# Performance work log

Hardware: AMD Instinct MI355X
Metric: run time of the kernel (lower is better)

## Reference

```python
import jax, jax.numpy as jnp
import numpy as np

B, H, W, C = 16, 32, 32, 512
L, CT = 77, 512
NH, HD = 8, 64
G = 32          # GroupNorm groups
EPS = 1e-6      # flax GroupNorm default epsilon
NEG = -1e10


def group_norm(x, scale, bias):
    # flax GroupNorm on [b, n, c]: stats over (n, channels-within-group) per (b, group)
    b, n, c = x.shape
    xg = x.reshape(b, n, G, c // G)
    mu = xg.mean(axis=(1, 3), keepdims=True)
    var = xg.var(axis=(1, 3), keepdims=True)
    xg = (xg - mu) * jax.lax.rsqrt(var + EPS)
    return xg.reshape(b, n, c) * scale + bias


def setup_inputs() -> dict:
    key = jax.random.key(0)
    ks = jax.random.split(key, 8)
    w = lambda k, shape: jax.random.normal(k, shape, jnp.float32) * 0.02
    return {
        "inputs": jax.random.normal(ks[0], (B, H, W, C), jnp.float32),
        "text_enc": jax.random.normal(ks[1], (B, L, CT), jnp.float32),
        "text_mask": jnp.ones((B, L), jnp.int32),
        "gn_q_scale": jnp.ones((C,), jnp.float32),
        "gn_q_bias": jnp.zeros((C,), jnp.float32),
        "gn_kv_scale": jnp.ones((C,), jnp.float32),
        "gn_kv_bias": jnp.zeros((C,), jnp.float32),
        "gn_t_scale": jnp.ones((CT,), jnp.float32),
        "gn_t_bias": jnp.zeros((CT,), jnp.float32),
        "Wq": w(ks[2], (C, NH, HD)),
        "Wk_self": w(ks[3], (C, NH, HD)),
        "Wv_self": w(ks[4], (C, NH, HD)),
        "Wk_cross": w(ks[5], (CT, NH, HD)),
        "Wv_cross": w(ks[6], (CT, NH, HD)),
        "Wout": w(ks[7], (NH, HD, C)),
    }


def reference(inputs, text_enc, text_mask,
              gn_q_scale, gn_q_bias, gn_kv_scale, gn_kv_bias,
              gn_t_scale, gn_t_bias,
              Wq, Wk_self, Wv_self, Wk_cross, Wv_cross, Wout):
    b, h, w, c = inputs.shape
    n = h * w
    x = inputs.reshape(b, n, c)

    x_q = group_norm(x, gn_q_scale, gn_q_bias)
    x_kv = group_norm(x, gn_kv_scale, gn_kv_bias)
    t = group_norm(text_enc, gn_t_scale, gn_t_bias)

    # q/k/v projections; fused: KV = concat(self-KV from image, cross-KV from text)
    scale = jnp.asarray(1.0 / np.sqrt(HD), inputs.dtype)
    q = jnp.einsum('bqc,chd->bqhd', x_q, Wq) * scale  # scale_attn_logits
    k = jnp.concatenate([jnp.einsum('bkc,chd->bkhd', x_kv, Wk_self),
                         jnp.einsum('blc,chd->blhd', t, Wk_cross)], axis=1)
    v = jnp.concatenate([jnp.einsum('bkc,chd->bkhd', x_kv, Wv_self),
                         jnp.einsum('blc,chd->blhd', t, Wv_cross)], axis=1)

    # make_attention_mask(ones[b,n], concat(ones[b,n], text_mask)) -> [b,1,n,n+l];
    # query mask is all ones so only the KV mask matters.
    kv_mask = jnp.concatenate(
        [jnp.ones((b, n), jnp.bool_), text_mask > 0], axis=1)  # [b, n+l]

    logits = jnp.einsum('bqhd,bkhd->bhqk', q, k)  # [b, nh, n, n+l]
    logits = jnp.where(kv_mask[:, None, None, :], logits, jnp.asarray(NEG, logits.dtype))
    probs = jax.nn.softmax(logits, axis=-1)
    attn = jnp.einsum('bhqk,bkhd->bqhd', probs, v)
    out = jnp.einsum('bqhd,hdc->bqc', attn, Wout)
    return out.reshape(b, h, w, c) + inputs
```

## Files before the change

kernel.cpp:

```cpp
#include <hip/hip_runtime.h>
#include <hip/hip_bf16.h>

typedef __hip_bfloat16 bf16;
typedef __attribute__((ext_vector_type(8))) short short8;
typedef __attribute__((ext_vector_type(4))) float f32x4;
typedef __attribute__((ext_vector_type(16))) float f32x16;
#define MFMA16(a, b, c) __builtin_amdgcn_mfma_f32_16x16x32_bf16(a, b, c, 0, 0, 0)
#define MFMA32(a, b, c) __builtin_amdgcn_mfma_f32_32x32x16_bf16(a, b, c, 0, 0, 0)

#define BB   16
#define CCH  512
#define NN   1024
#define LLT  77
#define LPAD 128
#define NHH  8
#define HDD  64
#define GGN  32
#define NKV  1101
#define KVP  1152

__device__ __forceinline__ unsigned short f2bu(float f){
  bf16 h = __float2bfloat16(f);
  return *reinterpret_cast<unsigned short*>(&h);
}

__device__ __forceinline__ unsigned pk2(float lo, float hi){
  unsigned r;
  asm("v_cvt_pk_bf16_f32 %0, %1, %2" : "=v"(r) : "v"(lo), "v"(hi));
  return r;
}

__device__ __forceinline__ float fexp2(float x){
  float r;
  asm("v_exp_f32 %0, %1" : "=v"(r) : "v"(x));
  return r;
}

__device__ __forceinline__ void pl32swap(unsigned &a, unsigned &b){
  asm("v_permlane32_swap_b32 %0, %1" : "+v"(a), "+v"(b));
}

__device__ __forceinline__ void gload16(const bf16* g, bf16* l){
  __builtin_amdgcn_global_load_lds(
      (const __attribute__((address_space(1))) unsigned int*)g,
      (__attribute__((address_space(3))) unsigned int*)l,
      16, 0, 0);
}

__global__ __launch_bounds__(256) void pre_kernel(
    const float* __restrict__ ximg, const float* __restrict__ xtxt,
    float* __restrict__ stats,
    const float* __restrict__ W0, const float* __restrict__ W1,
    const float* __restrict__ W2, const float* __restrict__ W3,
    const float* __restrict__ W4, const float* __restrict__ W5,
    bf16* __restrict__ Wt)
{
  __shared__ float sh1[256], sh2[256];
  __shared__ alignas(16) float Ws[64][68];

  if (blockIdx.x < 1024){
    int isimg = blockIdx.x < 512;
    int bid = blockIdx.x & 511;
    int b = bid >> 5, g = bid & 31;
    int npos = isimg ? NN : LLT;
    const float* xb = (isimg ? ximg : xtxt) + (size_t)b * npos * CCH + g * 16;
    int tot4 = npos * 4;
    float s = 0.f, s2 = 0.f;
    for (int e = threadIdx.x; e < tot4; e += 256){
      int n = e >> 2, cq = (e & 3) * 4;
      float4 v = *(const float4*)(xb + (size_t)n * CCH + cq);
      s  += v.x + v.y + v.z + v.w;
      s2 += v.x * v.x + v.y * v.y + v.z * v.z + v.w * v.w;
    }
    sh1[threadIdx.x] = s; sh2[threadIdx.x] = s2;
    __syncthreads();
    for (int off = 128; off > 0; off >>= 1){
      if (threadIdx.x < off){
        sh1[threadIdx.x] += sh1[threadIdx.x + off];
        sh2[threadIdx.x] += sh2[threadIdx.x + off];
      }
      __syncthreads();
    }
    if (threadIdx.x == 0){
      float inv = 1.f / (float)(npos * 16);
      float m = sh1[0] * inv;
      float var = sh2[0] * inv - m * m;
      float* mu = stats + (isimg ? 0 : 1024);
      mu[bid] = m;
      mu[512 + bid] = rsqrtf(var + 1e-6f);
    }
  } else {
    int i = blockIdx.x - 1024;
    int wsel = i >> 6;
    int rem  = i & 63;
    int n0 = (rem & 7) * 64, k0 = (rem >> 3) * 64;
    const float* W = wsel == 0 ? W0 : wsel == 1 ? W1 : wsel == 2 ? W2 :
                     wsel == 3 ? W3 : wsel == 4 ? W4 : W5;
    bf16* dst = Wt + (size_t)wsel * CCH * CCH;

    int r = threadIdx.x >> 2, c = (threadIdx.x & 3) * 16;
    const float* src = W + (size_t)(k0 + r) * CCH + n0 + c;
    *(float4*)&Ws[r][c]      = *(const float4*)(src);
    *(float4*)&Ws[r][c + 4]  = *(const float4*)(src + 4);
    *(float4*)&Ws[r][c + 8]  = *(const float4*)(src + 8);
    *(float4*)&Ws[r][c + 12] = *(const float4*)(src + 12);
    __syncthreads();

    int nr = threadIdx.x >> 2, kc = (threadIdx.x & 3) * 16;
    uint4 o0, o1;
    o0.x = pk2(Ws[kc + 0][nr],  Ws[kc + 1][nr]);
    o0.y = pk2(Ws[kc + 2][nr],  Ws[kc + 3][nr]);
    o0.z = pk2(Ws[kc + 4][nr],  Ws[kc + 5][nr]);
    o0.w = pk2(Ws[kc + 6][nr],  Ws[kc + 7][nr]);
    o1.x = pk2(Ws[kc + 8][nr],  Ws[kc + 9][nr]);
    o1.y = pk2(Ws[kc + 10][nr], Ws[kc + 11][nr]);
    o1.z = pk2(Ws[kc + 12][nr], Ws[kc + 13][nr]);
    o1.w = pk2(Ws[kc + 14][nr], Ws[kc + 15][nr]);
    bf16* d = dst + (size_t)(n0 + nr) * CCH + k0 + kc;
    *(uint4*)d = o0;
    *(uint4*)(d + 8) = o1;
  }
}

__global__ __launch_bounds__(256) void norm_all_kernel(
    const float* __restrict__ x, const float* __restrict__ t,
    const float* __restrict__ stats,
    const float* __restrict__ gqs, const float* __restrict__ gqb,
    const float* __restrict__ gks, const float* __restrict__ gkb,
    const float* __restrict__ gts, const float* __restrict__ gtb,
    bf16* __restrict__ Xq, bf16* __restrict__ Xkv, bf16* __restrict__ Tn)
{
  if (blockIdx.x < 4096){
    size_t e = ((size_t)blockIdx.x * 256 + threadIdx.x) * 8;
    int b  = (int)(e >> 19);
    int ch = (int)(e & 511);
    int g  = ch >> 4;
    float m = stats[b * GGN + g], r = stats[512 + b * GGN + g];
    float4 x0 = *(const float4*)(x + e);
    float4 x1 = *(const float4*)(x + e + 4);
    float4 sq0 = *(const float4*)(gqs + ch), sq1 = *(const float4*)(gqs + ch + 4);
    float4 bq0 = *(const float4*)(gqb + ch), bq1 = *(const float4*)(gqb + ch + 4);
    float4 sk0 = *(const float4*)(gks + ch), sk1 = *(const float4*)(gks + ch + 4);
    float4 bk0 = *(const float4*)(gkb + ch), bk1 = *(const float4*)(gkb + ch + 4);
    float xs[8] = {x0.x,x0.y,x0.z,x0.w,x1.x,x1.y,x1.z,x1.w};
    float sqv[8] = {sq0.x,sq0.y,sq0.z,sq0.w,sq1.x,sq1.y,sq1.z,sq1.w};
    float bqv[8] = {bq0.x,bq0.y,bq0.z,bq0.w,bq1.x,bq1.y,bq1.z,bq1.w};
    float skv[8] = {sk0.x,sk0.y,sk0.z,sk0.w,sk1.x,sk1.y,sk1.z,sk1.w};
    float bkv[8] = {bk0.x,bk0.y,bk0.z,bk0.w,bk1.x,bk1.y,bk1.z,bk1.w};
    float q[8], k[8];
    #pragma unroll
    for (int j = 0; j < 8; j++){
      float nx = (xs[j] - m) * r;
      q[j] = (nx * sqv[j] + bqv[j]) * 0.18033688f;
      k[j] = nx * skv[j] + bkv[j];
    }
    uint4 oq, ok;
    oq.x = pk2(q[0], q[1]); oq.y = pk2(q[2], q[3]);
    oq.z = pk2(q[4], q[5]); oq.w = pk2(q[6], q[7]);
    ok.x = pk2(k[0], k[1]); ok.y = pk2(k[2], k[3]);
    ok.z = pk2(k[4], k[5]); ok.w = pk2(k[6], k[7]);
    *(uint4*)(Xq + e)  = oq;
    *(uint4*)(Xkv + e) = ok;
  } else {
    size_t e = ((size_t)(blockIdx.x - 4096) * 256 + threadIdx.x) * 8;
    int b  = (int)(e >> 16);
    int rem = (int)(e & 65535);
    int l  = rem >> 9;
    int ch = rem & 511;
    uint4 o;
    if (l < LLT){
      int g = ch >> 4;
      float m = stats[1024 + b * GGN + g], r = stats[1536 + b * GGN + g];
      const float* src = t + ((size_t)b * LLT + l) * CCH + ch;
      float4 x0 = *(const float4*)src, x1 = *(const float4*)(src + 4);
      float4 s0 = *(const float4*)(gts + ch), s1 = *(const float4*)(gts + ch + 4);
      float4 b0 = *(const float4*)(gtb + ch), b1 = *(const float4*)(gtb + ch + 4);
      float xs[8] = {x0.x,x0.y,x0.z,x0.w,x1.x,x1.y,x1.z,x1.w};
      float sv[8] = {s0.x,s0.y,s0.z,s0.w,s1.x,s1.y,s1.z,s1.w};
      float bv[8] = {b0.x,b0.y,b0.z,b0.w,b1.x,b1.y,b1.z,b1.w};
      float w[8];
      #pragma unroll
      for (int j = 0; j < 8; j++) w[j] = (xs[j] - m) * r * sv[j] + bv[j];
      o.x = pk2(w[0], w[1]); o.y = pk2(w[2], w[3]);
      o.z = pk2(w[4], w[5]); o.w = pk2(w[6], w[7]);
    } else {
      o = make_uint4(0, 0, 0, 0);
    }
    *(uint4*)(Tn + e) = o;
  }
}

__global__ __launch_bounds__(256) void proj_all_mfma(
    const bf16* __restrict__ Xq, const bf16* __restrict__ Xkv,
    const bf16* __restrict__ Tn, const bf16* __restrict__ Wt,
    bf16* __restrict__ Qo, bf16* __restrict__ Ko, bf16* __restrict__ Vo)
{
  __shared__ alignas(16) char SHRAW[65536];
  const int tid  = threadIdx.x;
  const int wave = tid >> 6, lane = tid & 63;
  const int l16 = lane & 15, quad = lane >> 4;
  const int bx = blockIdx.x;

  if (bx < 1536){
    bf16 (*T)[4][64][64] = reinterpret_cast<bf16(*)[4][64][64]>(SHRAW);
    const int wr = wave >> 1, wc = wave & 1;
    const int ct = bx >> 7;
    const int rt = bx & 127;
    const int mat = ct >> 2;
    const int cm0 = (ct & 3) * 128;
    const int b  = rt >> 3;
    const int n0 = (rt & 7) * 128;

    const bf16* A  = (mat == 0) ? Xq : Xkv;
    const bf16* Bw = Wt + (size_t)mat * CCH * CCH + (size_t)cm0 * CCH;

    f32x4 acc[4][4];
    #pragma unroll
    for (int rf = 0; rf < 4; rf++)
      #pragma unroll
      for (int cf = 0; cf < 4; cf++) acc[rf][cf] = (f32x4){0.f,0.f,0.f,0.f};

    const int lrow = lane >> 3, lcol = (lane & 7) * 8;
    const bf16* srcbase = (wave < 2)
        ? A  + ((size_t)b * NN + n0 + wave * 64) * CCH
        : Bw + (size_t)((wave - 2) * 64) * CCH;

    #pragma unroll
    for (int c = 0; c < 8; c++)
      gload16(srcbase + (size_t)(c * 8 + lrow) * CCH + lcol, &T[0][wave][c * 8][0]);
    __syncthreads();

    int cur = 0;
    for (int kt = 0; kt < 8; kt++){
      if (kt < 7){
        const int kc = (kt + 1) * 64;
        #pragma unroll
        for (int c = 0; c < 8; c++)
          gload16(srcbase + (size_t)(c * 8 + lrow) * CCH + kc + lcol,
                  &T[cur ^ 1][wave][c * 8][0]);
      }

      short8 af[4][2];
      #pragma unroll
      for (int rf = 0; rf < 4; rf++){
        af[rf][0] = *(const short8*)&T[cur][wr][rf * 16 + l16][quad * 8];
        af[rf][1] = *(const short8*)&T[cur][wr][rf * 16 + l16][32 + quad * 8];
      }
      #pragma unroll
      for (int cf = 0; cf < 4; cf++){
        const short8 b0 = *(const short8*)&T[cur][2 + wc][cf * 16 + l16][quad * 8];
        const short8 b1 = *(const short8*)&T[cur][2 + wc][cf * 16 + l16][32 + quad * 8];
        #pragma unroll
        for (int rf = 0; rf < 4; rf++){
          acc[rf][cf] = MFMA16(af[rf][0], b0, acc[rf][cf]);
          acc[rf][cf] = MFMA16(af[rf][1], b1, acc[rf][cf]);
        }
      }
      __syncthreads();
      cur ^= 1;
    }

    const int h  = (cm0 + wc * 64) >> 6;
    const int nb = n0 + wr * 64;
    bf16 (*Tw)[64] = reinterpret_cast<bf16(*)[64]>(SHRAW + wave * 8192);

    if (mat < 2){
      bf16* Out = (mat == 0) ? Qo : Ko;
      const int stride = (mat == 0) ? NN : KVP;
      #pragma unroll
      for (int rf = 0; rf < 4; rf++)
        #pragma unroll
        for (int cf = 0; cf < 4; cf++)
          #pragma unroll
          for (int r = 0; r < 4; r++)
            Tw[rf * 16 + quad * 4 + r][cf * 16 + l16] =
                __float2bfloat16(acc[rf][cf][r]);
      const int rr = lane >> 2, cs = (lane & 3) * 16;
      #pragma unroll
      for (int k2 = 0; k2 < 4; k2++){
        const int row = rr + k2 * 16;
        bf16* od = Out + (((size_t)b * NHH + h) * stride + nb + row) * HDD + cs;
        *(uint4*)od       = *(const uint4*)&Tw[row][cs];
        *(uint4*)(od + 8) = *(const uint4*)&Tw[row][cs + 8];
      }
    } else {
      #pragma unroll
      for (int cf = 0; cf < 4; cf++)
        #pragma unroll
        for (int rf = 0; rf < 4; rf++)
          #pragma unroll
          for (int r = 0; r < 4; r++)
            Tw[cf * 16 + l16][rf * 16 + quad * 4 + r] =
                __float2bfloat16(acc[rf][cf][r]);
      __syncthreads();
      const int dl = lane >> 2, cseg = (lane & 3) * 16;
      #pragma unroll
      for (int k2 = 0; k2 < 4; k2++){
        const int d = dl + k2 * 16;
        bf16* vd = Vo + (((size_t)b * NHH + h) * HDD + d) * KVP + nb + cseg;
        *(uint4*)vd       = *(const uint4*)&Tw[d][cseg];
        *(uint4*)(vd + 8) = *(const uint4*)&Tw[d][cseg + 8];
      }
    }
  } else {
    bf16 (*At)[72] = reinterpret_cast<bf16(*)[72]>(SHRAW);
    bf16 (*Bk)[72] = reinterpret_cast<bf16(*)[72]>(SHRAW + 64 * 72 * 2);
    bf16 (*Bv)[72] = reinterpret_cast<bf16(*)[72]>(SHRAW + 2 * 64 * 72 * 2);
    const int i  = bx - 1536;
    const int h  = i & 7;
    const int l0 = ((i >> 3) & 1) * 64;
    const int b  = i >> 4;

    const bf16* Wkc = Wt + 3 * (size_t)CCH * CCH;
    const bf16* Wvc = Wt + 4 * (size_t)CCH * CCH;

    f32x4 sk[4], sv[4];
    #pragma unroll
    for (int nt = 0; nt < 4; nt++){
      sk[nt] = (f32x4){0.f,0.f,0.f,0.f};
      sv[nt] = (f32x4){0.f,0.f,0.f,0.f};
    }

    const int sr = tid >> 2, sc = (tid & 3) * 16;
    const bf16* p_a  = Tn  + ((size_t)b * LPAD + l0 + sr) * CCH + sc;
    const bf16* p_bk = Wkc + (size_t)(h * 64 + sr) * CCH + sc;
    const bf16* p_bv = Wvc + (size_t)(h * 64 + sr) * CCH + sc;

    uint4 ra0 = *(const uint4*)p_a,   ra1 = *(const uint4*)(p_a + 8);
    uint4 rk0 = *(const uint4*)p_bk,  rk1 = *(const uint4*)(p_bk + 8);
    uint4 rv0 = *(const uint4*)p_bv,  rv1 = *(const uint4*)(p_bv + 8);

    for (int kt = 0; kt < 8; kt++){
      *(uint4*)&At[sr][sc]     = ra0;  *(uint4*)&At[sr][sc + 8] = ra1;
      *(uint4*)&Bk[sr][sc]     = rk0;  *(uint4*)&Bk[sr][sc + 8] = rk1;
      *(uint4*)&Bv[sr][sc]     = rv0;  *(uint4*)&Bv[sr][sc + 8] = rv1;
      if (kt < 7){
        const int k1 = (kt + 1) * 64;
        ra0 = *(const uint4*)(p_a + k1);   ra1 = *(const uint4*)(p_a + k1 + 8);
        rk0 = *(const uint4*)(p_bk + k1);  rk1 = *(const uint4*)(p_bk + k1 + 8);
        rv0 = *(const uint4*)(p_bv + k1);  rv1 = *(const uint4*)(p_bv + k1 + 8);
      }
      __syncthreads();

      const short8 a0 = *(const short8*)&At[wave * 16 + l16][quad * 8];
      const short8 a1 = *(const short8*)&At[wave * 16 + l16][32 + quad * 8];
      #pragma unroll
      for (int nt = 0; nt < 4; nt++){
        const short8 bk0 = *(const short8*)&Bk[nt * 16 + l16][quad * 8];
        const short8 bk1 = *(const short8*)&Bk[nt * 16 + l16][32 + quad * 8];
        sk[nt] = MFMA16(a0, bk0, sk[nt]);
        sk[nt] = MFMA16(a1, bk1, sk[nt]);
        const short8 bv0 = *(const short8*)&Bv[nt * 16 + l16][quad * 8];
        const short8 bv1 = *(const short8*)&Bv[nt * 16 + l16][32 + quad * 8];
        sv[nt] = MFMA16(a0, bv0, sv[nt]);
        sv[nt] = MFMA16(a1, bv1, sv[nt]);
      }
      __syncthreads();
    }

    #pragma unroll
    for (int r = 0; r < 4; r++){
      int kvrow = NN + l0 + wave * 16 + quad * 4 + r;
      bf16* kd = Ko + (((size_t)b * NHH + h) * KVP + kvrow) * HDD + l16;
      #pragma unroll
      for (int nt = 0; nt < 4; nt++)
        kd[nt * 16] = __float2bfloat16(sk[nt][r]);
    }

    __syncthreads();
    #pragma unroll
    for (int nt = 0; nt < 4; nt++)
      #pragma unroll
      for (int r = 0; r < 4; r++)
        Bk[nt * 16 + l16][wave * 16 + quad * 4 + r] = __float2bfloat16(sv[nt][r]);
    __syncthreads();
    {
      int d = tid >> 2, c = (tid & 3) * 16;
      bf16* vd = Vo + (((size_t)b * NHH + h) * HDD + d) * KVP + NN + l0 + c;
      *(uint4*)vd       = *(const uint4*)&Bk[d][c];
      *(uint4*)(vd + 8) = *(const uint4*)&Bk[d][c + 8];
    }
  }
}

__global__ __launch_bounds__(256, 4) void attn_mfma_kernel(
    const bf16* __restrict__ Q, const bf16* __restrict__ K,
    const bf16* __restrict__ Vt, const int* __restrict__ tmask,
    bf16* __restrict__ Ao)
{
  const int tid  = threadIdx.x;
  const int wave = tid >> 6;
  const int lane = tid & 63;
  const int l31  = lane & 31;
  const int hi   = lane >> 5;
  const int bx = blockIdx.x;
  const int q0 = (bx >> 7) * 128;
  const int g  = bx & 127;
  const int h  = g & 7;
  const int b  = g >> 3;

  __shared__ alignas(16) bf16 KV[2][2][64][72];

  const bf16* qp = Q + (((size_t)b * NHH + h) * NN + q0 + wave * 32 + l31) * HDD + hi * 8;
  short8 qf[4];
  qf[0] = *(const short8*)(qp);
  qf[1] = *(const short8*)(qp + 16);
  qf[2] = *(const short8*)(qp + 32);
  qf[3] = *(const short8*)(qp + 48);

  union { unsigned u[4]; short8 s8; } ones;
  ones.u[0] = 0x3F803F80u; ones.u[1] = 0x3F803F80u;
  ones.u[2] = 0x3F803F80u; ones.u[3] = 0x3F803F80u;

  f32x16 zf;
  #pragma unroll
  for (int i = 0; i < 16; i++) zf[i] = 0.f;

  f32x16 o_acc[2], l_acc;
  #pragma unroll
  for (int dt = 0; dt < 2; dt++)
    #pragma unroll
    for (int i = 0; i < 16; i++) o_acc[dt][i] = 0.f;
  #pragma unroll
  for (int i = 0; i < 16; i++) l_acc[i] = 0.f;

  const size_t kbase = ((size_t)b * NHH + h) * KVP;
  const size_t vbase = ((size_t)b * NHH + h) * (size_t)HDD * KVP;

  const int sr = tid >> 2;
  const int sc = (tid & 3) * 16;
  const bf16* kp = K  + (kbase + sr) * HDD + sc;
  const bf16* vp = Vt + vbase + (size_t)sr * KVP + sc;

  uint4 kr0 = *(const uint4*)kp, kr1 = *(const uint4*)(kp + 8);
  uint4 vr0 = *(const uint4*)vp, vr1 = *(const uint4*)(vp + 8);
  *(uint4*)&KV[0][0][sr][sc]     = kr0;
  *(uint4*)&KV[0][0][sr][sc + 8] = kr1;
  *(uint4*)&KV[0][1][sr][sc]     = vr0;
  *(uint4*)&KV[0][1][sr][sc + 8] = vr1;
  kr0 = *(const uint4*)(kp + 4096); kr1 = *(const uint4*)(kp + 4096 + 8);
  vr0 = *(const uint4*)(vp + 64);   vr1 = *(const uint4*)(vp + 64 + 8);
  __syncthreads();

  for (int kt = 0; kt < 18; kt++){
    const int cur = kt & 1;
    if (kt + 1 < 18){
      *(uint4*)&KV[cur ^ 1][0][sr][sc]     = kr0;
      *(uint4*)&KV[cur ^ 1][0][sr][sc + 8] = kr1;
      *(uint4*)&KV[cur ^ 1][1][sr][sc]     = vr0;
      *(uint4*)&KV[cur ^ 1][1][sr][sc + 8] = vr1;
    }
    if (kt + 2 < 18){
      const size_t ko = (size_t)(kt + 2) * 4096;
      const int    vo = (kt + 2) * 64;
      kr0 = *(const uint4*)(kp + ko); kr1 = *(const uint4*)(kp + ko + 8);
      vr0 = *(const uint4*)(vp + vo); vr1 = *(const uint4*)(vp + vo + 8);
    }

    const bf16 (*Ks)[72] = KV[cur][0];
    const bf16 (*Vs)[72] = KV[cur][1];
    const int kv0 = kt * 64;

    #pragma unroll
    for (int t = 0; t < 2; t++){
      const short8 kf0 = *(const short8*)&Ks[t * 32 + l31][hi * 8];
      const short8 kf1 = *(const short8*)&Ks[t * 32 + l31][16 + hi * 8];
      const short8 kf2 = *(const short8*)&Ks[t * 32 + l31][32 + hi * 8];
      const short8 kf3 = *(const short8*)&Ks[t * 32 + l31][48 + hi * 8];
      __builtin_amdgcn_s_setprio(1);
      f32x16 s = MFMA32(kf0, qf[0], zf);
      s = MFMA32(kf1, qf[1], s);
      s = MFMA32(kf2, qf[2], s);
      s = MFMA32(kf3, qf[3], s);
      __builtin_amdgcn_s_setprio(0);

      if (kv0 + 64 > NN){
        #pragma unroll
        for (int r = 0; r < 16; r++){
          int idx = kv0 - NN + t * 32 + (r & 3) + 8 * (r >> 2) + 4 * hi;
          int ci = idx < LLT ? idx : LLT - 1;
          float rep = (idx < LLT)
                        ? (tmask[b * LLT + ci] > 0 ? 1e30f : -1e10f)
                        : -1e30f;
          s[r] = fminf(s[r], rep);
        }
      }

      #pragma unroll
      for (int r = 0; r < 16; r++) s[r] = fexp2(s[r]);

      unsigned w0 = pk2(s[0],  s[1]),  w1 = pk2(s[2],  s[3]);
      unsigned w2 = pk2(s[4],  s[5]),  w3 = pk2(s[6],  s[7]);
      unsigned w4 = pk2(s[8],  s[9]),  w5 = pk2(s[10], s[11]);
      unsigned w6 = pk2(s[12], s[13]), w7 = pk2(s[14], s[15]);
      pl32swap(w0, w2);
      pl32swap(w1, w3);
      pl32swap(w4, w6);
      pl32swap(w5, w7);
      union { unsigned u[4]; short8 s8; } pf0, pf1;
      pf0.u[0] = w0; pf0.u[1] = w1; pf0.u[2] = w2; pf0.u[3] = w3;
      pf1.u[0] = w4; pf1.u[1] = w5; pf1.u[2] = w6; pf1.u[3] = w7;

      const short8 vf00 = *(const short8*)&Vs[l31][t * 32 + hi * 8];
      const short8 vf01 = *(const short8*)&Vs[l31][t * 32 + 16 + hi * 8];
      const short8 vf10 = *(const short8*)&Vs[32 + l31][t * 32 + hi * 8];
      const short8 vf11 = *(const short8*)&Vs[32 + l31][t * 32 + 16 + hi * 8];

      __builtin_amdgcn_s_setprio(1);
      l_acc = MFMA32(pf0.s8, ones.s8, l_acc);
      l_acc = MFMA32(pf1.s8, ones.s8, l_acc);
      o_acc[0] = MFMA32(pf0.s8, vf00, o_acc[0]);
      o_acc[0] = MFMA32(pf1.s8, vf01, o_acc[0]);
      o_acc[1] = MFMA32(pf0.s8, vf10, o_acc[1]);
      o_acc[1] = MFMA32(pf1.s8, vf11, o_acc[1]);
      __builtin_amdgcn_s_setprio(0);
    }
    __syncthreads();
  }

  #pragma unroll
  for (int r = 0; r < 16; r++){
    const int ql = (r & 3) + 8 * (r >> 2) + 4 * hi;
    const float linv = 1.f / l_acc[r];
    const int n = q0 + wave * 32 + ql;
    bf16* dst = Ao + ((size_t)b * NN + n) * CCH + h * HDD + l31;
    dst[0]  = __float2bfloat16(o_acc[0][r] * linv);
    dst[32] = __float2bfloat16(o_acc[1][r] * linv);
  }
}

__global__ __launch_bounds__(256) void outproj_mfma(
    const bf16* __restrict__ A, const bf16* __restrict__ Wt,
    const float* __restrict__ resid, float* __restrict__ out)
{
  __shared__ alignas(16) char SH[36864];
  bf16 (*T)[64][64] = reinterpret_cast<bf16(*)[64][64]>(SH);
  const int tid  = threadIdx.x;
  const int wave = tid >> 6, lane = tid & 63;
  const int l16 = lane & 15, quad = lane >> 4;
  const int wr = wave >> 1, wc = wave & 1;
  const int bx = blockIdx.x;
  const int c0 = (bx >> 7) * 128;
  const int g0 = (bx & 127) * 128;

  const bf16* Bw = Wt + (size_t)5 * CCH * CCH + (size_t)c0 * CCH;

  f32x4 acc[4][4];
  #pragma unroll
  for (int rf = 0; rf < 4; rf++)
    #pragma unroll
    for (int cf = 0; cf < 4; cf++) acc[rf][cf] = (f32x4){0.f,0.f,0.f,0.f};

  const int lrow = lane >> 3, lcol = (lane & 7) * 8;
  const bf16* srcbase = (wave < 2)
      ? A  + ((size_t)g0 + wave * 64) * CCH
      : Bw + (size_t)((wave - 2) * 64) * CCH;

  for (int kt = 0; kt < 8; kt++){
    const int kc = kt * 64;
    #pragma unroll
    for (int c = 0; c < 8; c++){
      const bf16* g = srcbase + (size_t)(c * 8 + lrow) * CCH + kc + lcol;
      gload16(g, &T[wave][c * 8][0]);
    }
    __syncthreads();

    short8 af[4][2];
    #pragma unroll
    for (int rf = 0; rf < 4; rf++){
      af[rf][0] = *(const short8*)&T[wr][rf * 16 + l16][quad * 8];
      af[rf][1] = *(const short8*)&T[wr][rf * 16 + l16][32 + quad * 8];
    }
    #pragma unroll
    for (int cf = 0; cf < 4; cf++){
      const short8 b0 = *(const short8*)&T[2 + wc][cf * 16 + l16][quad * 8];
      const short8 b1 = *(const short8*)&T[2 + wc][cf * 16 + l16][32 + quad * 8];
      #pragma unroll
      for (int rf = 0; rf < 4; rf++){
        acc[rf][cf] = MFMA16(af[rf][0], b0, acc[rf][cf]);
        acc[rf][cf] = MFMA16(af[rf][1], b1, acc[rf][cf]);
      }
    }
    __syncthreads();
  }

  float (*Tf)[68] = reinterpret_cast<float(*)[68]>(SH + wave * 8704);
  const int cg = (lane & 15) * 4;
  #pragma unroll
  for (int hf = 0; hf < 2; hf++){
    #pragma unroll
    for (int rf = 0; rf < 2; rf++)
      #pragma unroll
      for (int cf = 0; cf < 4; cf++)
        #pragma unroll
        for (int r = 0; r < 4; r++)
          Tf[rf * 16 + quad * 4 + r][cf * 16 + l16] = acc[hf * 2 + rf][cf][r];
    #pragma unroll
    for (int k = 0; k < 8; k++){
      const int row32 = k * 4 + quad;
      const size_t grow = (size_t)g0 + wr * 64 + hf * 32 + row32;
      const int gcol = c0 + wc * 64 + cg;
      float4 v  = *(const float4*)&Tf[row32][cg];
      float4 rz = *(const float4*)&resid[grow * CCH + gcol];
      v.x += rz.x; v.y += rz.y; v.z += rz.z; v.w += rz.w;
      *(float4*)&out[grow * CCH + gcol] = v;
    }
    if (hf == 0){
      asm volatile("s_waitcnt lgkmcnt(0)" ::: "memory");
      __builtin_amdgcn_sched_barrier(0);
    }
  }
}

extern "C" void kernel_launch(void* const* d_in, const int* in_sizes, int n_in,
                              void* d_out, int out_size, void* d_ws, size_t ws_size,
                              hipStream_t stream)
{
  const float* x     = (const float*)d_in[0];
  const float* txt   = (const float*)d_in[1];
  const int*   tmask = (const int*)d_in[2];
  const float* gqs   = (const float*)d_in[3];
  const float* gqb   = (const float*)d_in[4];
  const float* gks   = (const float*)d_in[5];
  const float* gkb   = (const float*)d_in[6];
  const float* gts   = (const float*)d_in[7];
  const float* gtb   = (const float*)d_in[8];
  const float* Wq    = (const float*)d_in[9];
  const float* Wks   = (const float*)d_in[10];
  const float* Wvs   = (const float*)d_in[11];
  const float* Wkc   = (const float*)d_in[12];
  const float* Wvc   = (const float*)d_in[13];
  const float* Wout  = (const float*)d_in[14];

  float* stats = (float*)d_ws;
  bf16* WtAll = (bf16*)(stats + 2048);
  bf16* Xq  = WtAll + (size_t)6 * CCH * CCH;
  bf16* Xkv = Xq  + (size_t)BB * NN * CCH;
  bf16* Tn  = Xkv + (size_t)BB * NN * CCH;
  bf16* Qw  = Tn  + (size_t)BB * LPAD * CCH;
  bf16* Kw  = Qw  + (size_t)BB * NHH * NN * HDD;
  bf16* Vw  = Kw  + (size_t)BB * NHH * KVP * HDD;
  bf16* Aw  = Xq;

  pre_kernel<<<1408, 256, 0, stream>>>(
      x, txt, stats, Wq, Wks, Wvs, Wkc, Wvc, Wout, WtAll);
  norm_all_kernel<<<4608, 256, 0, stream>>>(
      x, txt, stats, gqs, gqb, gks, gkb, gts, gtb, Xq, Xkv, Tn);
  proj_all_mfma<<<1792, 256, 0, stream>>>(
      Xq, Xkv, Tn, WtAll, Qw, Kw, Vw);
  attn_mfma_kernel<<<1024, 256, 0, stream>>>(Qw, Kw, Vw, tmask, Aw);
  outproj_mfma<<<512, 256, 0, stream>>>(Aw, WtAll, x, (float*)d_out);
}
```

Measured before the change: 241.7 us.

## Fuse GroupNorm statistics and normalization into one kernel per group

Merges the stats pass and the elementwise normalize pass into a single kernel: each block computes its (batch, group) mean and rstd, then re-reads its group's slice and writes the bf16 Xq/Xkv/Tn outputs. This removes one kernel launch and the global stats round trip, and the second read of x is likely to hit cache. In exchange the normalize pass runs on only 512 blocks with strided 16-channel slices and 8-byte stores, which lowers parallelism and coalescing compared with the old 4096-block fully contiguous pass.

```diff
diff --git a/kernel.cpp b/kernel.cpp
--- a/kernel.cpp
+++ b/kernel.cpp
@@ -18,6 +18,7 @@
 #define GGN  32
 #define NKV  1101
 #define KVP  1152
+#define QSC  0.18033688f
 
 __device__ __forceinline__ unsigned short f2bu(float f){
   bf16 h = __float2bfloat16(f);
@@ -47,66 +48,121 @@
       16, 0, 0);
 }
 
-__global__ __launch_bounds__(256) void pre_kernel(
-    const float* __restrict__ ximg, const float* __restrict__ xtxt,
-    float* __restrict__ stats,
+__global__ __launch_bounds__(256) void gn_norm_kernel(
+    const float* __restrict__ x, const float* __restrict__ t,
+    const float* __restrict__ gqs, const float* __restrict__ gqb,
+    const float* __restrict__ gks, const float* __restrict__ gkb,
+    const float* __restrict__ gts, const float* __restrict__ gtb,
     const float* __restrict__ W0, const float* __restrict__ W1,
     const float* __restrict__ W2, const float* __restrict__ W3,
     const float* __restrict__ W4, const float* __restrict__ W5,
-    bf16* __restrict__ Wt)
+    bf16* __restrict__ Wt,
+    bf16* __restrict__ Xq, bf16* __restrict__ Xkv, bf16* __restrict__ Tn)
 {
-  __shared__ float sh1[256], sh2[256];
+  __shared__ float sh1[256], sh2[256], mr[2];
   __shared__ alignas(16) float Ws[64][68];
-
-  if (blockIdx.x < 1024){
-    int isimg = blockIdx.x < 512;
-    int bid = blockIdx.x & 511;
-    int b = bid >> 5, g = bid & 31;
-    int npos = isimg ? NN : LLT;
-    const float* xb = (isimg ? ximg : xtxt) + (size_t)b * npos * CCH + g * 16;
-    int tot4 = npos * 4;
+  const int tid = threadIdx.x;
+  const int bid = blockIdx.x;
+
+  if (bid < 512){
+    const int b = bid >> 5, g = bid & 31;
+    const float* xb = x + (size_t)b * NN * CCH + g * 16;
     float s = 0.f, s2 = 0.f;
-    for (int e = threadIdx.x; e < tot4; e += 256){
-      int n = e >> 2, cq = (e & 3) * 4;
+    for (int i = tid; i < 4096; i += 256){
+      const int n = i >> 2, cq = (i & 3) * 4;
       float4 v = *(const float4*)(xb + (size_t)n * CCH + cq);
       s  += v.x + v.y + v.z + v.w;
       s2 += v.x * v.x + v.y * v.y + v.z * v.z + v.w * v.w;
     }
-    sh1[threadIdx.x] = s; sh2[threadIdx.x] = s2;
+    sh1[tid] = s; sh2[tid] = s2;
     __syncthreads();
     for (int off = 128; off > 0; off >>= 1){
-      if (threadIdx.x < off){
-        sh1[threadIdx.x] += sh1[threadIdx.x + off];
-        sh2[threadIdx.x] += sh2[threadIdx.x + off];
-      }
+      if (tid < off){ sh1[tid] += sh1[tid + off]; sh2[tid] += sh2[tid + off]; }
       __syncthreads();
     }
-    if (threadIdx.x == 0){
-      float inv = 1.f / (float)(npos * 16);
-      float m = sh1[0] * inv;
-      float var = sh2[0] * inv - m * m;
-      float* mu = stats + (isimg ? 0 : 1024);
-      mu[bid] = m;
-      mu[512 + bid] = rsqrtf(var + 1e-6f);
+    if (tid == 0){
+      const float inv = 1.f / 16384.f;
+      const float m = sh1[0] * inv;
+      mr[0] = m;
+      mr[1] = rsqrtf(sh2[0] * inv - m * m + 1e-6f);
+    }
+    __syncthreads();
+    const float m = mr[0], r = mr[1];
+    const int ch0 = g * 16;
+    for (int i = tid; i < 4096; i += 256){
+      const int n = i >> 2, cq = (i & 3) * 4;
+      const int ch = ch0 + cq;
+      float4 v  = *(const float4*)(xb + (size_t)n * CCH + cq);
+      float4 sq = *(const float4*)(gqs + ch), bq = *(const float4*)(gqb + ch);
+      float4 sk = *(const float4*)(gks + ch), bk = *(const float4*)(gkb + ch);
+      const float n0 = (v.x - m) * r, n1 = (v.y - m) * r;
+      const float n2 = (v.z - m) * r, n3 = (v.w - m) * r;
+      uint2 oq, ok;
+      oq.x = pk2((n0 * sq.x + bq.x) * QSC, (n1 * sq.y + bq.y) * QSC);
+      oq.y = pk2((n2 * sq.z + bq.z) * QSC, (n3 * sq.w + bq.w) * QSC);
+      ok.x = pk2(n0 * sk.x + bk.x, n1 * sk.y + bk.y);
+      ok.y = pk2(n2 * sk.z + bk.z, n3 * sk.w + bk.w);
+      const size_t off = ((size_t)b * NN + n) * CCH + ch;
+      *(uint2*)(Xq  + off) = oq;
+      *(uint2*)(Xkv + off) = ok;
+    }
+  } else if (bid < 1024){
+    const int b = (bid - 512) >> 5, g = (bid - 512) & 31;
+    const float* tb = t + (size_t)b * LLT * CCH + g * 16;
+    float s = 0.f, s2 = 0.f;
+    for (int i = tid; i < 308; i += 256){
+      const int l = i >> 2, cq = (i & 3) * 4;
+      float4 v = *(const float4*)(tb + (size_t)l * CCH + cq);
+      s  += v.x + v.y + v.z + v.w;
+      s2 += v.x * v.x + v.y * v.y + v.z * v.z + v.w * v.w;
+    }
+    sh1[tid] = s; sh2[tid] = s2;
+    __syncthreads();
+    for (int off = 128; off > 0; off >>= 1){
+      if (tid < off){ sh1[tid] += sh1[tid + off]; sh2[tid] += sh2[tid + off]; }
+      __syncthreads();
+    }
+    if (tid == 0){
+      const float inv = 1.f / (float)(LLT * 16);
+      const float m = sh1[0] * inv;
+      mr[0] = m;
+      mr[1] = rsqrtf(sh2[0] * inv - m * m + 1e-6f);
+    }
+    __syncthreads();
+    const float m = mr[0], r = mr[1];
+    const int ch0 = g * 16;
+    for (int i = tid; i < 512; i += 256){
+      const int l = i >> 2, cq = (i & 3) * 4;
+      const int ch = ch0 + cq;
+      uint2 o;
+      if (l < LLT){
+        float4 v  = *(const float4*)(tb + (size_t)l * CCH + cq);
+        float4 sv = *(const float4*)(gts + ch), bv = *(const float4*)(gtb + ch);
+        o.x = pk2((v.x - m) * r * sv.x + bv.x, (v.y - m) * r * sv.y + bv.y);
+        o.y = pk2((v.z - m) * r * sv.z + bv.z, (v.w - m) * r * sv.w + bv.w);
+      } else {
+        o.x = 0u; o.y = 0u;
+      }
+      *(uint2*)(Tn + ((size_t)b * LPAD + l) * CCH + ch) = o;
     }
   } else {
-    int i = blockIdx.x - 1024;
-    int wsel = i >> 6;
-    int rem  = i & 63;
-    int n0 = (rem & 7) * 64, k0 = (rem >> 3) * 64;
+    const int i = bid - 1024;
+    const int wsel = i >> 6;
+    const int rem  = i & 63;
+    const int n0 = (rem & 7) * 64, k0 = (rem >> 3) * 64;
     const float* W = wsel == 0 ? W0 : wsel == 1 ? W1 : wsel == 2 ? W2 :
                      wsel == 3 ? W3 : wsel == 4 ? W4 : W5;
     bf16* dst = Wt + (size_t)wsel * CCH * CCH;
 
-    int r = threadIdx.x >> 2, c = (threadIdx.x & 3) * 16;
-    const float* src = W + (size_t)(k0 + r) * CCH + n0 + c;
-    *(float4*)&Ws[r][c]      = *(const float4*)(src);
-    *(float4*)&Ws[r][c + 4]  = *(const float4*)(src + 4);
-    *(float4*)&Ws[r][c + 8]  = *(const float4*)(src + 8);
-    *(float4*)&Ws[r][c + 12] = *(const float4*)(src + 12);
-    __syncthreads();
-
-    int nr = threadIdx.x >> 2, kc = (threadIdx.x & 3) * 16;
+    const int rr = tid >> 2, c = (tid & 3) * 16;
+    const float* src = W + (size_t)(k0 + rr) * CCH + n0 + c;
+    *(float4*)&Ws[rr][c]      = *(const float4*)(src);
+    *(float4*)&Ws[rr][c + 4]  = *(const float4*)(src + 4);
+    *(float4*)&Ws[rr][c + 8]  = *(const float4*)(src + 8);
+    *(float4*)&Ws[rr][c + 12] = *(const float4*)(src + 12);
+    __syncthreads();
+
+    const int nr = tid >> 2, kc = (tid & 3) * 16;
     uint4 o0, o1;
     o0.x = pk2(Ws[kc + 0][nr],  Ws[kc + 1][nr]);
     o0.y = pk2(Ws[kc + 2][nr],  Ws[kc + 3][nr]);
@@ -119,74 +175,6 @@
     bf16* d = dst + (size_t)(n0 + nr) * CCH + k0 + kc;
     *(uint4*)d = o0;
     *(uint4*)(d + 8) = o1;
-  }
-}
-
-__global__ __launch_bounds__(256) void norm_all_kernel(
-    const float* __restrict__ x, const float* __restrict__ t,
-    const float* __restrict__ stats,
-    const float* __restrict__ gqs, const float* __restrict__ gqb,
-    const float* __restrict__ gks, const float* __restrict__ gkb,
-    const float* __restrict__ gts, const float* __restrict__ gtb,
-    bf16* __restrict__ Xq, bf16* __restrict__ Xkv, bf16* __restrict__ Tn)
-{
-  if (blockIdx.x < 4096){
-    size_t e = ((size_t)blockIdx.x * 256 + threadIdx.x) * 8;
-    int b  = (int)(e >> 19);
-    int ch = (int)(e & 511);
-    int g  = ch >> 4;
-    float m = stats[b * GGN + g], r = stats[512 + b * GGN + g];
-    float4 x0 = *(const float4*)(x + e);
-    float4 x1 = *(const float4*)(x + e + 4);
-    float4 sq0 = *(const float4*)(gqs + ch), sq1 = *(const float4*)(gqs + ch + 4);
-    float4 bq0 = *(const float4*)(gqb + ch), bq1 = *(const float4*)(gqb + ch + 4);
-    float4 sk0 = *(const float4*)(gks + ch), sk1 = *(const float4*)(gks + ch + 4);
-    float4 bk0 = *(const float4*)(gkb + ch), bk1 = *(const float4*)(gkb + ch + 4);
-    float xs[8] = {x0.x,x0.y,x0.z,x0.w,x1.x,x1.y,x1.z,x1.w};
-    float sqv[8] = {sq0.x,sq0.y,sq0.z,sq0.w,sq1.x,sq1.y,sq1.z,sq1.w};
-    float bqv[8] = {bq0.x,bq0.y,bq0.z,bq0.w,bq1.x,bq1.y,bq1.z,bq1.w};
-    float skv[8] = {sk0.x,sk0.y,sk0.z,sk0.w,sk1.x,sk1.y,sk1.z,sk1.w};
-    float bkv[8] = {bk0.x,bk0.y,bk0.z,bk0.w,bk1.x,bk1.y,bk1.z,bk1.w};
-    float q[8], k[8];
-    #pragma unroll
-    for (int j = 0; j < 8; j++){
-      float nx = (xs[j] - m) * r;
-      q[j] = (nx * sqv[j] + bqv[j]) * 0.18033688f;
-      k[j] = nx * skv[j] + bkv[j];
-    }
-    uint4 oq, ok;
-    oq.x = pk2(q[0], q[1]); oq.y = pk2(q[2], q[3]);
-    oq.z = pk2(q[4], q[5]); oq.w = pk2(q[6], q[7]);
-    ok.x = pk2(k[0], k[1]); ok.y = pk2(k[2], k[3]);
-    ok.z = pk2(k[4], k[5]); ok.w = pk2(k[6], k[7]);
-    *(uint4*)(Xq + e)  = oq;
-    *(uint4*)(Xkv + e) = ok;
-  } else {
-    size_t e = ((size_t)(blockIdx.x - 4096) * 256 + threadIdx.x) * 8;
-    int b  = (int)(e >> 16);
-    int rem = (int)(e & 65535);
-    int l  = rem >> 9;
-    int ch = rem & 511;
-    uint4 o;
-    if (l < LLT){
-      int g = ch >> 4;
-      float m = stats[1024 + b * GGN + g], r = stats[1536 + b * GGN + g];
-      const float* src = t + ((size_t)b * LLT + l) * CCH + ch;
-      float4 x0 = *(const float4*)src, x1 = *(const float4*)(src + 4);
-      float4 s0 = *(const float4*)(gts + ch), s1 = *(const float4*)(gts + ch + 4);
-      float4 b0 = *(const float4*)(gtb + ch), b1 = *(const float4*)(gtb + ch + 4);
-      float xs[8] = {x0.x,x0.y,x0.z,x0.w,x1.x,x1.y,x1.z,x1.w};
-      float sv[8] = {s0.x,s0.y,s0.z,s0.w,s1.x,s1.y,s1.z,s1.w};
-      float bv[8] = {b0.x,b0.y,b0.z,b0.w,b1.x,b1.y,b1.z,b1.w};
-      float w[8];
-      #pragma unroll
-      for (int j = 0; j < 8; j++) w[j] = (xs[j] - m) * r * sv[j] + bv[j];
-      o.x = pk2(w[0], w[1]); o.y = pk2(w[2], w[3]);
-      o.z = pk2(w[4], w[5]); o.w = pk2(w[6], w[7]);
-    } else {
-      o = make_uint4(0, 0, 0, 0);
-    }
-    *(uint4*)(Tn + e) = o;
   }
 }
 
@@ -642,10 +630,9 @@
   bf16* Vw  = Kw  + (size_t)BB * NHH * KVP * HDD;
   bf16* Aw  = Xq;
 
-  pre_kernel<<<1408, 256, 0, stream>>>(
-      x, txt, stats, Wq, Wks, Wvs, Wkc, Wvc, Wout, WtAll);
-  norm_all_kernel<<<4608, 256, 0, stream>>>(
-      x, txt, stats, gqs, gqb, gks, gkb, gts, gtb, Xq, Xkv, Tn);
+  gn_norm_kernel<<<1408, 256, 0, stream>>>(
+      x, txt, gqs, gqb, gks, gkb, gts, gtb,
+      Wq, Wks, Wvs, Wkc, Wvc, Wout, WtAll, Xq, Xkv, Tn);
   proj_all_mfma<<<1792, 256, 0, stream>>>(
       Xq, Xkv, Tn, WtAll, Qw, Kw, Vw);
   attn_mfma_kernel<<<1024, 256, 0, stream>>>(Qw, Kw, Vw, tmask, Aw);
```

After: 259.6 us. 1.07x slower.
